# Kernel optimization log

Hardware: AMD Instinct MI355X
Metric: run time of the kernel (lower is better)

The kernel has to match this reference:

```python
import jax, jax.numpy as jnp
import numpy as np

B, S, D, H = 4, 4096, 1024, 128

def setup_inputs() -> dict:
    key = jax.random.key(0)
    ks = jax.random.split(key, 4)
    scale = 1.0 / np.sqrt(D)
    return {
        "x":  jax.random.normal(ks[0], (B, S, D), dtype=jnp.float32),
        "Wq": jax.random.normal(ks[1], (D, H), dtype=jnp.float32) * scale,
        "bq": jnp.zeros((H,), dtype=jnp.float32),
        "Wk": jax.random.normal(ks[2], (D, H), dtype=jnp.float32) * scale,
        "bk": jnp.zeros((H,), dtype=jnp.float32),
        "Wv": jax.random.normal(ks[3], (D, H), dtype=jnp.float32) * scale,
        "bv": jnp.zeros((H,), dtype=jnp.float32),
    }

def reference(x, Wq, bq, Wk, bk, Wv, bv):
    # q, k, v: [B, S, H]
    q = x @ Wq + bq
    k = x @ Wk + bk
    v = x @ Wv + bv
    inv_sqrt_h = 1.0 / jnp.sqrt(jnp.asarray(q.shape[-1], q.dtype))
    # scores: [B, S, S]
    scores = jnp.einsum('bqh,bkh->bqk', q, k) * inv_sqrt_h
    seq = q.shape[1]
    causal = jnp.tril(jnp.ones((seq, seq), dtype=bool))
    scores = jnp.where(causal, scores, jnp.asarray(-jnp.inf, scores.dtype))
    probs = jax.nn.softmax(scores, axis=-1)
    # dropout p=0.0 -> identity
    return jnp.einsum('bqk,bkh->bqh', probs, v)
```

## Files before the change

kernel.cpp:

```cpp
#include <hip/hip_runtime.h>
#include <hip/hip_bf16.h>

#define B_ 4
#define S_ 4096
#define D_ 1024
#define H_ 128

typedef _Float16 half8 __attribute__((ext_vector_type(8)));
typedef _Float16 half4v __attribute__((ext_vector_type(4)));
typedef float float4v __attribute__((ext_vector_type(4)));


__global__ __launch_bounds__(256) void k_cvt_w(const float* __restrict__ Wq,
                                               const float* __restrict__ Wk,
                                               const float* __restrict__ Wv,
                                               _Float16* __restrict__ WT) {
    const float* W = blockIdx.y == 0 ? Wq : (blockIdx.y == 1 ? Wk : Wv);
    int idx = blockIdx.x * 256 + threadIdx.x;
    int k = idx >> 7, n = idx & 127;
    WT[(size_t)blockIdx.y * (H_ * D_) + (size_t)n * D_ + k] = (_Float16)W[idx];
}

__global__ __launch_bounds__(256) void k_proj(const float* __restrict__ X,
                                              const _Float16* __restrict__ WT,
                                              const float* __restrict__ bq,
                                              const float* __restrict__ bk,
                                              const float* __restrict__ bv,
                                              _Float16* __restrict__ Qf,
                                              _Float16* __restrict__ Kz,
                                              _Float16* __restrict__ Vz) {
    __shared__ _Float16 As[128][72];
    __shared__ _Float16 Bs[128][72];

    const int t    = threadIdx.x;
    const int w    = blockIdx.y;
    const int m0   = blockIdx.x * 128;
    const int lane = t & 63, wid = t >> 6;
    const int lo   = lane & 15, hi = lane >> 4;
    const int wr   = wid >> 1, wc = wid & 1;

    const _Float16* Wt = WT + (size_t)w * (H_ * D_);

    float4v acc[4][4];
#pragma unroll
    for (int mt = 0; mt < 4; ++mt)
#pragma unroll
        for (int nt = 0; nt < 4; ++nt) acc[mt][nt] = {0.f, 0.f, 0.f, 0.f};

    for (int it = 0; it < 16; ++it) {
        const int k0 = it * 64;
        __syncthreads();
#pragma unroll
        for (int pass = 0; pass < 4; ++pass) {
            const int r = pass * 32 + (t >> 3);
            const int c = (t & 7) * 8;
            float4v a0 = *(const float4v*)(X + (size_t)(m0 + r) * D_ + k0 + c);
            float4v a1 = *(const float4v*)(X + (size_t)(m0 + r) * D_ + k0 + c + 4);
            half8 ha;
            ha[0] = (_Float16)a0[0]; ha[1] = (_Float16)a0[1];
            ha[2] = (_Float16)a0[2]; ha[3] = (_Float16)a0[3];
            ha[4] = (_Float16)a1[0]; ha[5] = (_Float16)a1[1];
            ha[6] = (_Float16)a1[2]; ha[7] = (_Float16)a1[3];
            *(half8*)(&As[r][c]) = ha;
            *(half8*)(&Bs[r][c]) = *(const half8*)(Wt + (size_t)r * D_ + k0 + c);
        }
        __syncthreads();
#pragma unroll
        for (int kk = 0; kk < 2; ++kk) {
            half8 af[4], bf[4];
#pragma unroll
            for (int mt = 0; mt < 4; ++mt)
                af[mt] = *(const half8*)(&As[wr * 64 + mt * 16 + lo][kk * 32 + hi * 8]);
#pragma unroll
            for (int nt = 0; nt < 4; ++nt)
                bf[nt] = *(const half8*)(&Bs[wc * 64 + nt * 16 + lo][kk * 32 + hi * 8]);
#pragma unroll
            for (int mt = 0; mt < 4; ++mt)
#pragma unroll
                for (int nt = 0; nt < 4; ++nt)
                    acc[mt][nt] = __builtin_amdgcn_mfma_f32_16x16x32_f16(
                        af[mt], bf[nt], acc[mt][nt], 0, 0, 0);
        }
    }

    const float* bias = (w == 0) ? bq : ((w == 1) ? bk : bv);
    const float scale = (w == 0) ? (0.08838834764831845f * 1.4426950408889634f) : 1.0f;
#pragma unroll
    for (int mt = 0; mt < 4; ++mt)
#pragma unroll
        for (int nt = 0; nt < 4; ++nt) {
            const int n     = wc * 64 + nt * 16 + lo;
            const float bn  = bias[n];
            const int mbase = m0 + wr * 64 + mt * 16 + 4 * hi;
            if (w == 2) {
                const int bb = mbase >> 12;
                const int s0 = mbase & (S_ - 1);
                const int tt = s0 >> 5, h8 = (s0 >> 3) & 3, e0 = s0 & 7;
                const int hc = n >> 4, l2 = n & 15;
                half4v hv;
#pragma unroll
                for (int j = 0; j < 4; ++j) hv[j] = (_Float16)(acc[mt][nt][j] + bn);
                *(half4v*)(Vz + (size_t)(bb * 128 + tt) * 4096 + hc * 512 +
                           (h8 * 16 + l2) * 8 + e0) = hv;
            } else if (w == 1) {
#pragma unroll
                for (int j = 0; j < 4; ++j) {
                    const int row = mbase + j;
                    const int bb = row >> 12;
                    const int s  = row & (S_ - 1);
                    const int tt = s >> 5, r = s & 31;
                    const int c  = (r >> 2) & 1;
                    const int l2 = ((r >> 3) << 2) | (r & 3);
                    const int k2 = n >> 5, h2 = (n >> 3) & 3, e2 = n & 7;
                    Kz[(size_t)(bb * 128 + tt) * 4096 + (k2 * 2 + c) * 512 +
                       (h2 * 16 + l2) * 8 + e2] = (_Float16)(acc[mt][nt][j] + bn);
                }
            } else {
#pragma unroll
                for (int j = 0; j < 4; ++j)
                    Qf[(size_t)(mbase + j) * H_ + n] =
                        (_Float16)((acc[mt][nt][j] + bn) * scale);
            }
        }
}

__global__ __launch_bounds__(512, 2) void k_attn(const _Float16* __restrict__ Qf,
                                                 const _Float16* __restrict__ Kz,
                                                 const _Float16* __restrict__ Vz,
                                                 float* __restrict__ Out) {
    __shared__ float    sm_l[8][32];
    __shared__ _Float16 sm_o[8][32][136];

    const int t    = threadIdx.x;
    const int lane = t & 63, wid = t >> 6;
    const int lo = lane & 15, hi = lane >> 4;

    const int i   = blockIdx.x;
    const int b   = (i >> 1) & 3;
    const int qtr = ((i >> 3) << 1) | (i & 1);
    const int qt  = (qtr < 64) ? qtr : (191 - qtr);
    const int q0  = qt << 5;

    const _Float16* Qb = Qf + (size_t)b * (S_ * H_);
    const _Float16* Kb = Kz + (size_t)b * 524288;
    const _Float16* Vb = Vz + (size_t)b * 524288;

    half8 qfa[4], qfb[4];
#pragma unroll
    for (int kk = 0; kk < 4; ++kk) {
        qfa[kk] = *(const half8*)(Qb + (size_t)(q0 + lo) * H_ + kk * 32 + hi * 8);
        qfb[kk] = *(const half8*)(Qb + (size_t)(q0 + 16 + lo) * H_ + kk * 32 + hi * 8);
    }

    float4v oa[8], ob[8];
#pragma unroll
    for (int hc = 0; hc < 8; ++hc) { oa[hc] = {0.f,0.f,0.f,0.f}; ob[hc] = {0.f,0.f,0.f,0.f}; }
    float la = 0.f, lb = 0.f;

    const int lane8 = lane * 8;
    const int ntiles = qt + 1;

    half8 kc0[4], kc1[4];
    if (wid < ntiles) {
        const _Float16* Kt = Kb + (size_t)wid * 4096 + lane8;
#pragma unroll
        for (int kk = 0; kk < 4; ++kk) {
            kc0[kk] = *(const half8*)(Kt + (kk * 2    ) * 512);
            kc1[kk] = *(const half8*)(Kt + (kk * 2 + 1) * 512);
        }
    }

    for (int tt = wid; tt < ntiles; tt += 8) {
        const _Float16* Vt = Vb + (size_t)tt * 4096 + lane8;
        half8 vf[8];
#pragma unroll
        for (int hc = 0; hc < 8; ++hc)
            vf[hc] = *(const half8*)(Vt + hc * 512);
        const int tn = (tt + 8 < ntiles) ? (tt + 8) : tt;
        half8 kn0[4], kn1[4];
        {
            const _Float16* Ktn = Kb + (size_t)tn * 4096 + lane8;
#pragma unroll
            for (int kk = 0; kk < 4; ++kk) {
                kn0[kk] = *(const half8*)(Ktn + (kk * 2    ) * 512);
                kn1[kk] = *(const half8*)(Ktn + (kk * 2 + 1) * 512);
            }
        }
        float4v s0a = {0.f,0.f,0.f,0.f}, s1a = {0.f,0.f,0.f,0.f};
        float4v s0b = {0.f,0.f,0.f,0.f}, s1b = {0.f,0.f,0.f,0.f};
#pragma unroll
        for (int kk = 0; kk < 4; ++kk) {
            s0a = __builtin_amdgcn_mfma_f32_16x16x32_f16(kc0[kk], qfa[kk], s0a, 0, 0, 0);
            s0b = __builtin_amdgcn_mfma_f32_16x16x32_f16(kc0[kk], qfb[kk], s0b, 0, 0, 0);
            s1a = __builtin_amdgcn_mfma_f32_16x16x32_f16(kc1[kk], qfa[kk], s1a, 0, 0, 0);
            s1b = __builtin_amdgcn_mfma_f32_16x16x32_f16(kc1[kk], qfb[kk], s1b, 0, 0, 0);
        }
        if (tt == qt) {
#pragma unroll
            for (int j = 0; j < 4; ++j) {
                const int c0 = 8 * hi + j, c1 = 8 * hi + 4 + j;
                if (c0 > lo)      s0a[j] = -INFINITY;
                if (c1 > lo)      s1a[j] = -INFINITY;
                if (c0 > 16 + lo) s0b[j] = -INFINITY;
                if (c1 > 16 + lo) s1b[j] = -INFINITY;
            }
        }
        float pa0 = __builtin_amdgcn_exp2f(s0a[0]), pa1 = __builtin_amdgcn_exp2f(s0a[1]);
        float pa2 = __builtin_amdgcn_exp2f(s0a[2]), pa3 = __builtin_amdgcn_exp2f(s0a[3]);
        float pa4 = __builtin_amdgcn_exp2f(s1a[0]), pa5 = __builtin_amdgcn_exp2f(s1a[1]);
        float pa6 = __builtin_amdgcn_exp2f(s1a[2]), pa7 = __builtin_amdgcn_exp2f(s1a[3]);
        float pb0 = __builtin_amdgcn_exp2f(s0b[0]), pb1 = __builtin_amdgcn_exp2f(s0b[1]);
        float pb2 = __builtin_amdgcn_exp2f(s0b[2]), pb3 = __builtin_amdgcn_exp2f(s0b[3]);
        float pb4 = __builtin_amdgcn_exp2f(s1b[0]), pb5 = __builtin_amdgcn_exp2f(s1b[1]);
        float pb6 = __builtin_amdgcn_exp2f(s1b[2]), pb7 = __builtin_amdgcn_exp2f(s1b[3]);
        la += ((pa0+pa1)+(pa2+pa3)) + ((pa4+pa5)+(pa6+pa7));
        lb += ((pb0+pb1)+(pb2+pb3)) + ((pb4+pb5)+(pb6+pb7));
        half8 pfa, pfb;
        pfa[0]=(_Float16)pa0; pfa[1]=(_Float16)pa1; pfa[2]=(_Float16)pa2; pfa[3]=(_Float16)pa3;
        pfa[4]=(_Float16)pa4; pfa[5]=(_Float16)pa5; pfa[6]=(_Float16)pa6; pfa[7]=(_Float16)pa7;
        pfb[0]=(_Float16)pb0; pfb[1]=(_Float16)pb1; pfb[2]=(_Float16)pb2; pfb[3]=(_Float16)pb3;
        pfb[4]=(_Float16)pb4; pfb[5]=(_Float16)pb5; pfb[6]=(_Float16)pb6; pfb[7]=(_Float16)pb7;
#pragma unroll
        for (int hc = 0; hc < 8; ++hc) {
            oa[hc] = __builtin_amdgcn_mfma_f32_16x16x32_f16(vf[hc], pfa, oa[hc], 0, 0, 0);
            ob[hc] = __builtin_amdgcn_mfma_f32_16x16x32_f16(vf[hc], pfb, ob[hc], 0, 0, 0);
        }
#pragma unroll
        for (int kk = 0; kk < 4; ++kk) { kc0[kk] = kn0[kk]; kc1[kk] = kn1[kk]; }
    }

    la += __shfl_xor(la, 16); la += __shfl_xor(la, 32);
    lb += __shfl_xor(lb, 16); lb += __shfl_xor(lb, 32);

    sm_l[wid][lo]      = la;
    sm_l[wid][16 + lo] = lb;
#pragma unroll
    for (int hc = 0; hc < 8; ++hc) {
        half4v va, vb;
#pragma unroll
        for (int j = 0; j < 4; ++j) { va[j] = (_Float16)oa[hc][j]; vb[j] = (_Float16)ob[hc][j]; }
        *(half4v*)(&sm_o[wid][lo][hc * 16 + 4 * hi])      = va;
        *(half4v*)(&sm_o[wid][16 + lo][hc * 16 + 4 * hi]) = vb;
    }
    __syncthreads();

#pragma unroll
    for (int qh = 0; qh < 2; ++qh) {
        const int q = qh * 16 + lo;
        float L = 0.f;
#pragma unroll
        for (int w = 0; w < 8; ++w) L += sm_l[w][q];
        const float invL = 1.f / L;
        float4v ov = {0.f, 0.f, 0.f, 0.f};
#pragma unroll
        for (int w = 0; w < 8; ++w) {
            half4v tv = *(const half4v*)(&sm_o[w][q][wid * 16 + 4 * hi]);
#pragma unroll
            for (int j = 0; j < 4; ++j) ov[j] += (float)tv[j];
        }
#pragma unroll
        for (int j = 0; j < 4; ++j) ov[j] *= invL;
        *(float4v*)(Out + ((size_t)b * S_ + q0 + q) * H_ + wid * 16 + 4 * hi) = ov;
    }
}

extern "C" void kernel_launch(void* const* d_in, const int* in_sizes, int n_in,
                              void* d_out, int out_size, void* d_ws, size_t ws_size,
                              hipStream_t stream) {
    const float* x  = (const float*)d_in[0];
    const float* Wq = (const float*)d_in[1];
    const float* bq = (const float*)d_in[2];
    const float* Wk = (const float*)d_in[3];
    const float* bk = (const float*)d_in[4];
    const float* Wv = (const float*)d_in[5];
    const float* bv = (const float*)d_in[6];
    float* out = (float*)d_out;

    char* ws = (char*)d_ws;
    _Float16* WT = (_Float16*)ws;
    _Float16* Qf = (_Float16*)(ws + 786432);
    _Float16* Kz = (_Float16*)(ws + 786432 + 4194304);
    _Float16* Vz = (_Float16*)(ws + 786432 + 8388608);

    hipLaunchKernelGGL(k_cvt_w, dim3(512, 3), dim3(256), 0, stream, Wq, Wk, Wv, WT);
    hipLaunchKernelGGL(k_proj, dim3(128, 3), dim3(256), 0, stream,
                       x, WT, bq, bk, bv, Qf, Kz, Vz);
    hipLaunchKernelGGL(k_attn, dim3(512), dim3(512), 0, stream, Qf, Kz, Vz, out);
}
```

Measured before the change: 65.13 us.

## Halve projection M-tile and stage outputs through LDS for coalesced stores

The projection kernel's M tile shrinks from 128 to 64 rows, so the grid grows from 384 to 768 blocks with a flat index. Launch bounds now request 3 blocks per CU, which should fill the 256 CUs better. The epilogue writes biased and scaled results into shared memory first, then stores Q, K and V in their swizzled layouts as coalesced 16-byte vectors instead of scattered 2-byte writes. The cost is that each weight tile is reused across fewer rows, so global W traffic doubles, and the epilogue adds extra LDS work and barriers.

```diff
diff --git a/kernel.cpp b/kernel.cpp
--- a/kernel.cpp
+++ b/kernel.cpp
@@ -21,61 +21,77 @@
     WT[(size_t)blockIdx.y * (H_ * D_) + (size_t)n * D_ + k] = (_Float16)W[idx];
 }
 
-__global__ __launch_bounds__(256) void k_proj(const float* __restrict__ X,
-                                              const _Float16* __restrict__ WT,
-                                              const float* __restrict__ bq,
-                                              const float* __restrict__ bk,
-                                              const float* __restrict__ bv,
-                                              _Float16* __restrict__ Qf,
-                                              _Float16* __restrict__ Kz,
-                                              _Float16* __restrict__ Vz) {
-    __shared__ _Float16 As[128][72];
-    __shared__ _Float16 Bs[128][72];
+__global__ __launch_bounds__(256, 3) void k_proj(const float* __restrict__ X,
+                                                 const _Float16* __restrict__ WT,
+                                                 const float* __restrict__ bq,
+                                                 const float* __restrict__ bk,
+                                                 const float* __restrict__ bv,
+                                                 _Float16* __restrict__ Qf,
+                                                 _Float16* __restrict__ Kz,
+                                                 _Float16* __restrict__ Vz) {
+    __shared__ _Float16 smem[(64 + 128) * 72];
+    _Float16* As = smem;
+    _Float16* Bs = smem + 64 * 72;
 
     const int t    = threadIdx.x;
-    const int w    = blockIdx.y;
-    const int m0   = blockIdx.x * 128;
+    const int bid  = blockIdx.x;
+    const int w    = bid >> 8;
+    const int m0   = (bid & 255) * 64;
     const int lane = t & 63, wid = t >> 6;
     const int lo   = lane & 15, hi = lane >> 4;
     const int wr   = wid >> 1, wc = wid & 1;
 
     const _Float16* Wt = WT + (size_t)w * (H_ * D_);
 
-    float4v acc[4][4];
-#pragma unroll
-    for (int mt = 0; mt < 4; ++mt)
+    const int ar = t >> 2, ac = (t & 3) * 16;
+    const int br = t >> 1, bc = (t & 1) * 32;
+
+    float4v acc[2][4];
+#pragma unroll
+    for (int mt = 0; mt < 2; ++mt)
 #pragma unroll
         for (int nt = 0; nt < 4; ++nt) acc[mt][nt] = {0.f, 0.f, 0.f, 0.f};
 
     for (int it = 0; it < 16; ++it) {
         const int k0 = it * 64;
         __syncthreads();
-#pragma unroll
-        for (int pass = 0; pass < 4; ++pass) {
-            const int r = pass * 32 + (t >> 3);
-            const int c = (t & 7) * 8;
-            float4v a0 = *(const float4v*)(X + (size_t)(m0 + r) * D_ + k0 + c);
-            float4v a1 = *(const float4v*)(X + (size_t)(m0 + r) * D_ + k0 + c + 4);
-            half8 ha;
-            ha[0] = (_Float16)a0[0]; ha[1] = (_Float16)a0[1];
-            ha[2] = (_Float16)a0[2]; ha[3] = (_Float16)a0[3];
-            ha[4] = (_Float16)a1[0]; ha[5] = (_Float16)a1[1];
-            ha[6] = (_Float16)a1[2]; ha[7] = (_Float16)a1[3];
-            *(half8*)(&As[r][c]) = ha;
-            *(half8*)(&Bs[r][c]) = *(const half8*)(Wt + (size_t)r * D_ + k0 + c);
+        {
+            const float* xp = X + (size_t)(m0 + ar) * D_ + k0 + ac;
+            float4v x0 = *(const float4v*)(xp);
+            float4v x1 = *(const float4v*)(xp + 4);
+            float4v x2 = *(const float4v*)(xp + 8);
+            float4v x3 = *(const float4v*)(xp + 12);
+            half8 h0, h1;
+            h0[0]=(_Float16)x0[0]; h0[1]=(_Float16)x0[1]; h0[2]=(_Float16)x0[2]; h0[3]=(_Float16)x0[3];
+            h0[4]=(_Float16)x1[0]; h0[5]=(_Float16)x1[1]; h0[6]=(_Float16)x1[2]; h0[7]=(_Float16)x1[3];
+            h1[0]=(_Float16)x2[0]; h1[1]=(_Float16)x2[1]; h1[2]=(_Float16)x2[2]; h1[3]=(_Float16)x2[3];
+            h1[4]=(_Float16)x3[0]; h1[5]=(_Float16)x3[1]; h1[6]=(_Float16)x3[2]; h1[7]=(_Float16)x3[3];
+            *(half8*)(&As[ar * 72 + ac])     = h0;
+            *(half8*)(&As[ar * 72 + ac + 8]) = h1;
+        }
+        {
+            const _Float16* wp = Wt + (size_t)br * D_ + k0 + bc;
+            half8 b0 = *(const half8*)(wp);
+            half8 b1 = *(const half8*)(wp + 8);
+            half8 b2 = *(const half8*)(wp + 16);
+            half8 b3 = *(const half8*)(wp + 24);
+            *(half8*)(&Bs[br * 72 + bc])      = b0;
+            *(half8*)(&Bs[br * 72 + bc + 8])  = b1;
+            *(half8*)(&Bs[br * 72 + bc + 16]) = b2;
+            *(half8*)(&Bs[br * 72 + bc + 24]) = b3;
         }
         __syncthreads();
 #pragma unroll
         for (int kk = 0; kk < 2; ++kk) {
-            half8 af[4], bf[4];
-#pragma unroll
-            for (int mt = 0; mt < 4; ++mt)
-                af[mt] = *(const half8*)(&As[wr * 64 + mt * 16 + lo][kk * 32 + hi * 8]);
+            half8 af[2], bf[4];
+#pragma unroll
+            for (int mt = 0; mt < 2; ++mt)
+                af[mt] = *(const half8*)(&As[(wr * 32 + mt * 16 + lo) * 72 + kk * 32 + hi * 8]);
 #pragma unroll
             for (int nt = 0; nt < 4; ++nt)
-                bf[nt] = *(const half8*)(&Bs[wc * 64 + nt * 16 + lo][kk * 32 + hi * 8]);
-#pragma unroll
-            for (int mt = 0; mt < 4; ++mt)
+                bf[nt] = *(const half8*)(&Bs[(wc * 64 + nt * 16 + lo) * 72 + kk * 32 + hi * 8]);
+#pragma unroll
+            for (int mt = 0; mt < 2; ++mt)
 #pragma unroll
                 for (int nt = 0; nt < 4; ++nt)
                     acc[mt][nt] = __builtin_amdgcn_mfma_f32_16x16x32_f16(
@@ -85,43 +101,55 @@
 
     const float* bias = (w == 0) ? bq : ((w == 1) ? bk : bv);
     const float scale = (w == 0) ? (0.08838834764831845f * 1.4426950408889634f) : 1.0f;
-#pragma unroll
-    for (int mt = 0; mt < 4; ++mt)
+    __syncthreads();
+    _Float16* Ct = smem;
+#pragma unroll
+    for (int mt = 0; mt < 2; ++mt)
 #pragma unroll
         for (int nt = 0; nt < 4; ++nt) {
-            const int n     = wc * 64 + nt * 16 + lo;
-            const float bn  = bias[n];
-            const int mbase = m0 + wr * 64 + mt * 16 + 4 * hi;
-            if (w == 2) {
-                const int bb = mbase >> 12;
-                const int s0 = mbase & (S_ - 1);
-                const int tt = s0 >> 5, h8 = (s0 >> 3) & 3, e0 = s0 & 7;
-                const int hc = n >> 4, l2 = n & 15;
-                half4v hv;
-#pragma unroll
-                for (int j = 0; j < 4; ++j) hv[j] = (_Float16)(acc[mt][nt][j] + bn);
-                *(half4v*)(Vz + (size_t)(bb * 128 + tt) * 4096 + hc * 512 +
-                           (h8 * 16 + l2) * 8 + e0) = hv;
-            } else if (w == 1) {
-#pragma unroll
-                for (int j = 0; j < 4; ++j) {
-                    const int row = mbase + j;
-                    const int bb = row >> 12;
-                    const int s  = row & (S_ - 1);
-                    const int tt = s >> 5, r = s & 31;
-                    const int c  = (r >> 2) & 1;
-                    const int l2 = ((r >> 3) << 2) | (r & 3);
-                    const int k2 = n >> 5, h2 = (n >> 3) & 3, e2 = n & 7;
-                    Kz[(size_t)(bb * 128 + tt) * 4096 + (k2 * 2 + c) * 512 +
-                       (h2 * 16 + l2) * 8 + e2] = (_Float16)(acc[mt][nt][j] + bn);
-                }
-            } else {
-#pragma unroll
-                for (int j = 0; j < 4; ++j)
-                    Qf[(size_t)(mbase + j) * H_ + n] =
-                        (_Float16)((acc[mt][nt][j] + bn) * scale);
-            }
-        }
+            const int col   = wc * 64 + nt * 16 + lo;
+            const float bn  = bias[col];
+            const int rbase = wr * 32 + mt * 16 + 4 * hi;
+#pragma unroll
+            for (int j = 0; j < 4; ++j)
+                Ct[(rbase + j) * 136 + col] = (_Float16)((acc[mt][nt][j] + bn) * scale);
+        }
+    __syncthreads();
+
+    const int bb  = m0 >> 12;
+    const int tt0 = (m0 & (S_ - 1)) >> 5;
+
+    if (w == 0) {
+        const int r = t >> 2, c0 = (t & 3) * 32;
+        _Float16* dst = Qf + (size_t)(m0 + r) * H_ + c0;
+        const _Float16* srcp = &Ct[r * 136 + c0];
+#pragma unroll
+        for (int cc = 0; cc < 4; ++cc)
+            *(half8*)(dst + cc * 8) = *(const half8*)(srcp + cc * 8);
+    } else if (w == 1) {
+        const int rowp = ((lo >> 2) << 3) + (lo & 3);
+#pragma unroll
+        for (int q = 0; q < 4; ++q) {
+            const int fid = wid * 4 + q;
+            const int ft = fid >> 3, k2 = (fid >> 1) & 3, c = fid & 1;
+            const int row = ft * 32 + rowp + 4 * c;
+            half8 v = *(const half8*)(&Ct[row * 136 + k2 * 32 + hi * 8]);
+            *(half8*)(Kz + (size_t)(bb * 128 + tt0 + ft) * 4096 +
+                      (k2 * 2 + c) * 512 + lane * 8) = v;
+        }
+    } else {
+#pragma unroll
+        for (int q = 0; q < 4; ++q) {
+            const int fid = wid * 4 + q;
+            const int ft = fid >> 3, hc = fid & 7;
+            half8 v;
+#pragma unroll
+            for (int e = 0; e < 8; ++e)
+                v[e] = Ct[(ft * 32 + hi * 8 + e) * 136 + hc * 16 + lo];
+            *(half8*)(Vz + (size_t)(bb * 128 + tt0 + ft) * 4096 +
+                      hc * 512 + lane * 8) = v;
+        }
+    }
 }
 
 __global__ __launch_bounds__(512, 2) void k_attn(const _Float16* __restrict__ Qf,
@@ -283,7 +311,7 @@
     _Float16* Vz = (_Float16*)(ws + 786432 + 8388608);
 
     hipLaunchKernelGGL(k_cvt_w, dim3(512, 3), dim3(256), 0, stream, Wq, Wk, Wv, WT);
-    hipLaunchKernelGGL(k_proj, dim3(128, 3), dim3(256), 0, stream,
+    hipLaunchKernelGGL(k_proj, dim3(768), dim3(256), 0, stream,
                        x, WT, bq, bk, bv, Qf, Kz, Vz);
     hipLaunchKernelGGL(k_attn, dim3(512), dim3(512), 0, stream, Qf, Kz, Vz, out);
 }
```

New measurement: 68.17 us. +4.7%, slower.
